# Kernel optimization log

Measured on AMD Instinct MI355X. Metric: run time of the kernel, lower is better.

Reference implementation:

```python
import jax, jax.numpy as jnp
import numpy as np

N, E, G = 50000, 800000, 64
IN, HID, T, EDGE_DIM, HLS = 32, 64, 2, 2, 32
# deg histogram: all nodes degree 16 -> avg_deg['log'] = log(16+1)
AVG_LOG = float(np.log(17.0))


def _pna(x, src, dst, eattr, We, be, Wpre, bpre, Wpost, bpost, Wlin, blin):
    """PNAConv with aggregators [mean,min,max,std], scalers [identity,amp,att],
    towers=T, pre_layers=1, post_layers=1, divide_input=False."""
    n, F = x.shape
    enc = eattr @ We + be                                   # [E, F] edge encoder
    # message: concat(x_i, x_j, edge) -> per-tower Linear(3F -> F)
    h = jnp.concatenate([x[dst], x[src], enc], axis=-1)     # [E, 3F] (same for all towers)
    m = jnp.einsum('ef,tfo->eto', h, Wpre) + bpre           # [E, T, F]
    ones = jnp.ones((m.shape[0],), m.dtype)
    cnt = jax.ops.segment_sum(ones, dst, num_segments=n)    # in-degree [N]
    d = jnp.maximum(cnt, 1.0)[:, None, None]
    s = jax.ops.segment_sum(m, dst, num_segments=n)
    mean = s / d
    msq = jax.ops.segment_sum(m * m, dst, num_segments=n) / d
    std = jnp.sqrt(jax.nn.relu(msq - mean * mean) + 1e-5)
    has = (cnt > 0)[:, None, None]
    mn = jnp.where(has, jax.ops.segment_min(m, dst, num_segments=n), 0.0)
    mx = jnp.where(has, jax.ops.segment_max(m, dst, num_segments=n), 0.0)
    agg = jnp.concatenate([mean, mn, mx, std], axis=-1)     # [N, T, 4F]
    logd = jnp.log(d + 1.0)
    scaled = jnp.concatenate([agg, agg * (logd / AVG_LOG), agg * (AVG_LOG / logd)], axis=-1)  # [N,T,12F]
    xt = jnp.broadcast_to(x[:, None, :], (n, Wpre.shape[0], F))
    out = jnp.concatenate([xt, scaled], axis=-1)            # [N, T, 13F]
    o = jnp.einsum('nti,tio->nto', out, Wpost) + bpost      # [N, T, F_out]
    return o.reshape(n, -1) @ Wlin + blin                   # [N, HID]


def setup_inputs():
    key = jax.random.key(0)
    ks = iter(jax.random.split(key, 48))
    def p(shape):
        return jax.random.normal(next(ks), shape, jnp.float32) * 0.05
    inp = {}
    inp['x'] = jax.random.normal(next(ks), (N, IN), jnp.float32)
    inp['edge_attr'] = jax.random.normal(next(ks), (E, EDGE_DIM), jnp.float32)
    inp['hls_attr'] = jax.random.normal(next(ks), (G, HLS), jnp.float32)
    inp['edge_index'] = jax.random.randint(next(ks), (2, E), 0, N)
    inp['batch'] = jnp.sort(jax.random.randint(next(ks), (N,), 0, G))
    Fo = HID // T
    for l, Fin in enumerate([IN, HID]):
        inp[f'We{l}'] = p((EDGE_DIM, Fin)); inp[f'be{l}'] = jnp.zeros((Fin,), jnp.float32)
        inp[f'Wpre{l}'] = p((T, 3 * Fin, Fin)); inp[f'bpre{l}'] = jnp.zeros((T, Fin), jnp.float32)
        inp[f'Wpost{l}'] = p((T, 13 * Fin, Fo)); inp[f'bpost{l}'] = jnp.zeros((T, Fo), jnp.float32)
        inp[f'Wlin{l}'] = p((HID, HID)); inp[f'blin{l}'] = jnp.zeros((HID,), jnp.float32)
    inp['W1'] = p((HID + HLS, 64)); inp['b1'] = jnp.zeros((64,), jnp.float32)
    inp['W2'] = p((64, 64)); inp['b2'] = jnp.zeros((64,), jnp.float32)
    inp['W3'] = p((64, 1)); inp['b3'] = jnp.zeros((1,), jnp.float32)
    return inp


def reference(x, edge_attr, hls_attr,
              We0, be0, Wpre0, bpre0, Wpost0, bpost0, Wlin0, blin0,
              We1, be1, Wpre1, bpre1, Wpost1, bpost1, Wlin1, blin1,
              W1, b1, W2, b2, W3, b3,
              edge_index, batch):
    src, dst = edge_index[0], edge_index[1]
    h = jax.nn.relu(_pna(x, src, dst, edge_attr, We0, be0, Wpre0, bpre0, Wpost0, bpost0, Wlin0, blin0))
    h = jax.nn.relu(_pna(h, src, dst, edge_attr, We1, be1, Wpre1, bpre1, Wpost1, bpost1, Wlin1, blin1))
    g = jax.ops.segment_sum(h, batch, num_segments=G)       # global_add_pool [G, HID]
    g = jnp.concatenate([g, hls_attr], axis=-1)
    g = jax.nn.relu(g @ W1 + b1)
    g = jax.nn.relu(g @ W2 + b2)
    return g @ W3 + b3                                      # [G, 1]
```

## Files before the change

### kernel.cpp

```cpp
#include <hip/hip_runtime.h>
#include <math.h>
#include <float.h>

#define NN 50000
#define EE 800000
#define CAP 64

#define NB 196
#define SPAN 256
#define BCAP 4608

typedef unsigned short ushort_t;
typedef short short8 __attribute__((ext_vector_type(8)));
typedef float floatx4 __attribute__((ext_vector_type(4)));

__device__ __constant__ float kAVG_LOG = 2.8332133440562162f;

__device__ inline ushort_t f2bf(float v) {
    union { float f; unsigned u; } x; x.f = v;
    unsigned r = x.u + 0x7fffu + ((x.u >> 16) & 1u);
    return (ushort_t)(r >> 16);
}
__device__ inline float bf2f(ushort_t b) {
    union { unsigned u; float f; } x; x.u = ((unsigned)b) << 16; return x.f;
}
__device__ inline float bitsf(unsigned u) {
    union { unsigned u; float f; } x; x.u = u; return x.f;
}
__device__ inline void splitbf(float v, ushort_t& hi, ushort_t& lo) {
    hi = f2bf(v);
    lo = f2bf(v - bf2f(hi));
}

template <int F>
__device__ void prep_ab_dev(const float* __restrict__ We, const float* __restrict__ be,
                            const float* __restrict__ Wpre, const float* __restrict__ bpre,
                            float* __restrict__ U, float* __restrict__ Wab,
                            float* __restrict__ bias_ab) {
    const int TF = 2 * F;
    int tid = threadIdx.x;
    for (int idx = tid; idx < 2 * TF; idx += 256) {
        int c = idx / TF, f = idx % TF;
        int t = f / F, o = f % F;
        float s = 0.f;
        for (int g = 0; g < F; ++g)
            s += We[c * F + g] * Wpre[((size_t)t * 3 * F + 2 * F + g) * F + o];
        U[idx] = s;
    }
    for (int idx = tid; idx < F * 2 * TF; idx += 256) {
        int g = idx / (2 * TF), cc = idx % (2 * TF);
        int t, o, row;
        if (cc < TF) { t = cc / F; o = cc % F; row = g; }
        else { int c2 = cc - TF; t = c2 / F; o = c2 % F; row = F + g; }
        Wab[idx] = Wpre[((size_t)t * 3 * F + row) * F + o];
    }
    for (int cc = tid; cc < 2 * TF; cc += 256) {
        float v = 0.f;
        if (cc < TF) {
            int t = cc / F, o = cc % F;
            float s = 0.f;
            for (int g = 0; g < F; ++g)
                s += be[g] * Wpre[((size_t)t * 3 * F + 2 * F + g) * F + o];
            v = s + bpre[t * F + o];
        }
        bias_ab[cc] = v;
    }
}

template <int F>
__device__ void prep_zf_elem(int idx, const float* __restrict__ Wpost, const float* __restrict__ Wlin,
                             ushort_t* __restrict__ Bh, ushort_t* __restrict__ Bl) {
    const int KT = 9 * F;
    int jg = idx / KT, k = idx - jg * KT;
    int b = jg >> 6, j = jg & 63;
    float v = 0.f;
    if (k < F) {
        if (b == 0) {
#pragma unroll
            for (int t = 0; t < 2; ++t)
#pragma unroll
                for (int c = 0; c < 32; ++c)
                    v += Wpost[((size_t)t * 13 * F + k) * 32 + c] * Wlin[(t * 32 + c) * 64 + j];
        }
    } else {
        int r = k - F;
        int t = r / (4 * F), rr = r - t * 4 * F;
#pragma unroll
        for (int c = 0; c < 32; ++c)
            v += Wpost[((size_t)t * 13 * F + F + b * 4 * F + rr) * 32 + c] * Wlin[(t * 32 + c) * 64 + j];
    }
    ushort_t h_, l_;
    splitbf(v, h_, l_);
    Bh[(size_t)jg * KT + k] = h_;
    Bl[(size_t)jg * KT + k] = l_;
}

#define NZ0 216
#define NZ1 432
#define PREPB (NZ0 + NZ1 + 3)
#define INITB 6250

__global__ __launch_bounds__(256) void prep_init(
    const float* We0, const float* be0, const float* Wpre0, const float* bpre0,
    const float* Wpost0, const float* Wlin0, const float* bpost0, const float* blin0,
    const float* We1, const float* be1, const float* Wpre1, const float* bpre1,
    const float* Wpost1, const float* Wlin1, const float* bpost1, const float* blin1,
    float* U0, float* Wab0, float* bias_ab0, ushort_t* Bh0, ushort_t* Bl0, float* bias_zf0,
    float* U1, float* Wab1, float* bias_ab1, ushort_t* Bh1, ushort_t* Bl1, float* bias_zf1,
    int* gcount, float* pool, const float* __restrict__ x, ushort_t* __restrict__ xb) {
    int b = blockIdx.x;
    int tid = threadIdx.x;
    if (b >= PREPB) {
        int i = (b - PREPB) * 256 + tid;
        if (i < NN * 32) xb[i] = f2bf(x[i]);
        if (i < NB) gcount[i] = 0;
        if (i < 64 * 64) pool[i] = 0.f;
        return;
    }
    if (b < NZ0) {
        prep_zf_elem<32>(b * 256 + tid, Wpost0, Wlin0, Bh0, Bl0);
    } else if (b < NZ0 + NZ1) {
        prep_zf_elem<64>((b - NZ0) * 256 + tid, Wpost1, Wlin1, Bh1, Bl1);
    } else if (b == NZ0 + NZ1) {
        prep_ab_dev<32>(We0, be0, Wpre0, bpre0, U0, Wab0, bias_ab0);
    } else if (b == NZ0 + NZ1 + 1) {
        prep_ab_dev<64>(We1, be1, Wpre1, bpre1, U1, Wab1, bias_ab1);
    } else {
        for (int j = tid; j < 64; j += 256) {
            float s0 = blin0[j], s1 = blin1[j];
#pragma unroll
            for (int t = 0; t < 2; ++t)
#pragma unroll
                for (int c = 0; c < 32; ++c) {
                    s0 += bpost0[t * 32 + c] * Wlin0[(t * 32 + c) * 64 + j];
                    s1 += bpost1[t * 32 + c] * Wlin1[(t * 32 + c) * 64 + j];
                }
            bias_zf0[j] = s0;
            bias_zf1[j] = s1;
        }
    }
}

__global__ __launch_bounds__(1024) void partition_edges(
    const int* __restrict__ ei, const float* __restrict__ ea,
    int* __restrict__ gcount, uint2* __restrict__ part) {
    __shared__ int hist[NB];
    __shared__ int lbase[NB];
    int tid = threadIdx.x;
    int e0 = blockIdx.x * 4096;
    for (int i = tid; i < NB; i += 1024) hist[i] = 0;
    __syncthreads();
    int bq[4], rnk[4];
    unsigned px[4], py[4];
#pragma unroll
    for (int q = 0; q < 4; ++q) {
        int e = e0 + q * 1024 + tid;
        bq[q] = -1;
        if (e < EE) {
            int s = ei[e];
            int d = ei[EE + e];
            float2 v = *(const float2*)(ea + 2 * e);
            bq[q] = d >> 8;
            px[q] = ((unsigned)(d & 255) << 16) | (unsigned)s;
            py[q] = ((unsigned)f2bf(v.y) << 16) | (unsigned)f2bf(v.x);
            rnk[q] = atomicAdd(&hist[bq[q]], 1);
        }
    }
    __syncthreads();
    for (int i = tid; i < NB; i += 1024)
        lbase[i] = atomicAdd(&gcount[i], hist[i]);
    __syncthreads();
#pragma unroll
    for (int q = 0; q < 4; ++q) {
        if (bq[q] >= 0) {
            int slot = lbase[bq[q]] + rnk[q];
            if (slot < BCAP)
                part[(size_t)bq[q] * BCAP + slot] = make_uint2(px[q], py[q]);
        }
    }
}

__device__ void csr_fill_block(int g, const int* __restrict__ gcount,
                               const uint2* __restrict__ part,
                               int* __restrict__ cnt, uint2* __restrict__ csr) {
    __shared__ int lcnt[SPAN];
    int tid = threadIdx.x;
    lcnt[tid] = 0;
    __syncthreads();
    int total = gcount[g];
    if (total > BCAP) total = BCAP;
    size_t pbase = (size_t)g * BCAP;
    for (int i = tid; i < total; i += 256) {
        uint2 rec = part[pbase + i];
        int rel = rec.x >> 16;
        int src = rec.x & 0xffff;
        int p = atomicAdd(&lcnt[rel], 1);
        if (p < CAP) {
            int node = (g << 8) + rel;
            csr[(size_t)node * CAP + p] = make_uint2((unsigned)src, rec.y);
        }
    }
    __syncthreads();
    int node = (g << 8) + tid;
    if (node < NN) cnt[node] = lcnt[tid];
}

__device__ void gemm_bias_block(const float* __restrict__ A, const float* __restrict__ B,
                                const float* __restrict__ bias, float* __restrict__ Ca,
                                ushort_t* __restrict__ Cb, int M, int K, int Ncols, int bstart,
                                int mb, int cb) {
    __shared__ float As[32][132];
    __shared__ float Bs[32][68];
    int m0 = mb * 128, c0 = cb * 64;
    int tid = threadIdx.x;
    int tx = tid & 15, ty = tid >> 4;
    int ms = tid >> 3, u = tid & 7;
    float acc[8][4] = {};
    for (int k0 = 0; k0 < K; k0 += 32) {
#pragma unroll
        for (int p = 0; p < 4; ++p) {
            int m = ms + 32 * p;
            int gm = m0 + m;
            float4 v = make_float4(0.f, 0.f, 0.f, 0.f);
            if (gm < M) v = *(const float4*)(A + (size_t)gm * K + k0 + u * 4);
            As[u * 4 + 0][m] = v.x; As[u * 4 + 1][m] = v.y;
            As[u * 4 + 2][m] = v.z; As[u * 4 + 3][m] = v.w;
        }
#pragma unroll
        for (int p = 0; p < 2; ++p) {
            int idx = tid + 256 * p;
            int kk = idx >> 4, q = idx & 15;
            *(float4*)&Bs[kk][q * 4] = *(const float4*)(B + (size_t)(k0 + kk) * Ncols + c0 + q * 4);
        }
        __syncthreads();
#pragma unroll 8
        for (int k = 0; k < 32; ++k) {
            float a0[8], b0[4];
            *(float4*)&a0[0] = *(const float4*)&As[k][ty * 8];
            *(float4*)&a0[4] = *(const float4*)&As[k][ty * 8 + 4];
            *(float4*)&b0[0] = *(const float4*)&Bs[k][tx * 4];
#pragma unroll
            for (int i = 0; i < 8; ++i)
#pragma unroll
                for (int j = 0; j < 4; ++j) acc[i][j] = fmaf(a0[i], b0[j], acc[i][j]);
        }
        __syncthreads();
    }
    float bj[4];
#pragma unroll
    for (int j = 0; j < 4; ++j) bj[j] = bias[c0 + tx * 4 + j];
    bool bside = (c0 >= bstart);
    int TFw = bstart;
#pragma unroll
    for (int i = 0; i < 8; ++i) {
        int gm = m0 + ty * 8 + i;
        if (gm >= M) continue;
        float v0 = acc[i][0] + bj[0], v1 = acc[i][1] + bj[1];
        float v2 = acc[i][2] + bj[2], v3 = acc[i][3] + bj[3];
        if (!bside) {
            *(float4*)(Ca + (size_t)gm * TFw + c0 + tx * 4) = make_float4(v0, v1, v2, v3);
        } else {
            ushort4 w;
            w.x = f2bf(v0); w.y = f2bf(v1); w.z = f2bf(v2); w.w = f2bf(v3);
            *(ushort4*)(Cb + (size_t)gm * TFw + (c0 - bstart) + tx * 4) = w;
        }
    }
}

__global__ __launch_bounds__(256) void gemm_bias(const float* __restrict__ A, const float* __restrict__ B,
                                                 const float* __restrict__ bias, float* __restrict__ Ca,
                                                 ushort_t* __restrict__ Cb, int M, int K, int Ncols, int bstart) {
    gemm_bias_block(A, B, bias, Ca, Cb, M, K, Ncols, bstart, blockIdx.x, blockIdx.y);
}

__global__ __launch_bounds__(256) void csr_gemm0(
    const int* __restrict__ gcount, const uint2* __restrict__ part,
    int* __restrict__ cnt, uint2* __restrict__ csr,
    const float* __restrict__ A, const float* __restrict__ B, const float* __restrict__ bias,
    float* __restrict__ Ca, ushort_t* __restrict__ Cb) {
    int bx = blockIdx.x;
    if (bx % 5 == 0) {
        csr_fill_block(bx / 5, gcount, part, cnt, csr);
    } else {
        int idx = bx - 1 - bx / 5;
        gemm_bias_block(A, B, bias, Ca, Cb, NN, 32, 128, 64, idx % 391, idx / 391);
    }
}

template <int F>
__global__ __launch_bounds__(256) void aggregate(const float* __restrict__ ABa, const ushort_t* __restrict__ ABb,
                                                 const int* __restrict__ cnt, const uint2* __restrict__ csr,
                                                 const float* __restrict__ U,
                                                 ushort_t* __restrict__ agg_b, float2* __restrict__ sc) {
    const int TF = 2 * F;
    const int FPL = TF / 64;
    int lane = threadIdx.x & 63;
    int n = blockIdx.x * 4 + (threadIdx.x >> 6);
    if (n >= NN) return;
    int f0 = FPL * lane;

    float base[FPL], u0[FPL], u1[FPL], sum[FPL], sq[FPL], mn[FPL], mx[FPL];
#pragma unroll
    for (int r = 0; r < FPL; ++r) {
        base[r] = ABa[(size_t)n * TF + f0 + r];
        u0[r] = U[f0 + r];
        u1[r] = U[TF + f0 + r];
        sum[r] = 0.f; sq[r] = 0.f; mn[r] = FLT_MAX; mx[r] = -FLT_MAX;
    }
    int deg = cnt[n];
    int ec = deg < CAP ? deg : CAP;
    if (ec > 0) {
        int ebase = n * CAP;
        int myi = lane < ec ? lane : ec - 1;
        uint2 ent = csr[ebase + myi];
        int msrc = (int)ent.x;
        unsigned mea = ent.y;
        int e = 0;
        for (; e + 8 <= ec; e += 8) {
            int sb[8]; unsigned ep[8];
            unsigned wv[8];
#pragma unroll
            for (int i = 0; i < 8; ++i) {
                sb[i] = __shfl(msrc, e + i);
                ep[i] = (unsigned)__shfl((int)mea, e + i);
            }
#pragma unroll
            for (int i = 0; i < 8; ++i) {
                if constexpr (FPL == 2)
                    wv[i] = *(const unsigned*)(ABb + (size_t)sb[i] * TF + f0);
                else
                    wv[i] = ABb[(size_t)sb[i] * TF + f0];
            }
#pragma unroll
            for (int i = 0; i < 8; ++i) {
                float ex = bitsf(ep[i] << 16);
                float ey = bitsf(ep[i] & 0xffff0000u);
                float v[FPL];
                if constexpr (FPL == 2) {
                    v[0] = bitsf(wv[i] << 16);
                    v[1] = bitsf(wv[i] & 0xffff0000u);
                } else {
                    v[0] = bitsf(wv[i] << 16);
                }
#pragma unroll
                for (int r = 0; r < FPL; ++r) {
                    float q = fmaf(ex, u0[r], fmaf(ey, u1[r], v[r]));
                    sum[r] += q;
                    sq[r] = fmaf(q, q, sq[r]);
                    mn[r] = fminf(mn[r], q);
                    mx[r] = fmaxf(mx[r], q);
                }
            }
        }
        if (e < ec) {
            int sb[8]; unsigned ep[8];
            unsigned wv[8];
#pragma unroll
            for (int i = 0; i < 8; ++i) {
                sb[i] = __shfl(msrc, e + i);
                ep[i] = (unsigned)__shfl((int)mea, e + i);
            }
#pragma unroll
            for (int i = 0; i < 8; ++i) {
                if (e + i < ec) {
                    if constexpr (FPL == 2)
                        wv[i] = *(const unsigned*)(ABb + (size_t)sb[i] * TF + f0);
                    else
                        wv[i] = ABb[(size_t)sb[i] * TF + f0];
                }
            }
#pragma unroll
            for (int i = 0; i < 8; ++i) {
                if (e + i < ec) {
                    float ex = bitsf(ep[i] << 16);
                    float ey = bitsf(ep[i] & 0xffff0000u);
                    float v[FPL];
                    if constexpr (FPL == 2) {
                        v[0] = bitsf(wv[i] << 16);
                        v[1] = bitsf(wv[i] & 0xffff0000u);
                    } else {
                        v[0] = bitsf(wv[i] << 16);
                    }
#pragma unroll
                    for (int r = 0; r < FPL; ++r) {
                        float q = fmaf(ex, u0[r], fmaf(ey, u1[r], v[r]));
                        sum[r] += q;
                        sq[r] = fmaf(q, q, sq[r]);
                        mn[r] = fminf(mn[r], q);
                        mx[r] = fmaxf(mx[r], q);
                    }
                }
            }
        }
    }
    float d = (float)(deg > 1 ? deg : 1);
    float inv_d = 1.f / d;
    bool has = deg > 0;
#pragma unroll
    for (int r = 0; r < FPL; ++r) {
        float mean_q = sum[r] * inv_d;
        float var = sq[r] * inv_d - mean_q * mean_q;
        float stdv = sqrtf(fmaxf(var, 0.f) + 1e-5f);
        float mean = has ? base[r] + mean_q : 0.f;
        float vmn = has ? base[r] + mn[r] : 0.f;
        float vmx = has ? base[r] + mx[r] : 0.f;
        int f = f0 + r;
        int t = f / F, o = f - t * F;
        size_t rowb = (size_t)n * (4 * TF) + (size_t)t * (4 * F);
        agg_b[rowb + o] = f2bf(mean);
        agg_b[rowb + F + o] = f2bf(vmn);
        agg_b[rowb + 2 * F + o] = f2bf(vmx);
        agg_b[rowb + 3 * F + o] = f2bf(stdv);
    }
    if (lane == 0) {
        float logd = logf(d + 1.f);
        sc[n] = make_float2(logd / kAVG_LOG, kAVG_LOG / logd);
    }
}

template <int F, bool POOL>
__global__ __launch_bounds__(256, 2) void gemm_zf(
    const ushort_t* __restrict__ xs_b, const ushort_t* __restrict__ agg_b,
    const ushort_t* __restrict__ Bh, const ushort_t* __restrict__ Bl,
    const float* __restrict__ bias_zf, const float2* __restrict__ sc,
    float* __restrict__ H, ushort_t* __restrict__ H_b,
    const int* __restrict__ batch, float* __restrict__ pool) {
    const int KT = 9 * F;
    extern __shared__ char smem[];
    ushort_t* A_s  = (ushort_t*)smem;
    ushort_t* Bh_s = A_s + 128 * 40;
    ushort_t* Bl_s = Bh_s + 192 * 40;
    float* hbuf = (float*)smem;

    int m0 = blockIdx.x * 128;
    int tid = threadIdx.x;
    int lane = tid & 63;
    int wave = tid >> 6;
    int ln = lane & 15, quad = lane >> 4;

    floatx4 acc[8][3];
#pragma unroll
    for (int i = 0; i < 8; ++i)
#pragma unroll
        for (int j = 0; j < 3; ++j) acc[i][j] = (floatx4)(0.f);

    int arow = tid >> 2, asg = tid & 3;
    int bcol[3], bsg[3];
#pragma unroll
    for (int p = 0; p < 3; ++p) {
        int idx = tid + 256 * p;
        bcol[p] = idx >> 2;
        bsg[p] = idx & 3;
    }

    const short8 zero8 = {0, 0, 0, 0, 0, 0, 0, 0};
    short8 pa[2], pbh[3], pbl[3];
    {
        int c0 = asg * 8;
#pragma unroll
        for (int q = 0; q < 2; ++q) {
            int gm = m0 + arow + q * 64;
            pa[q] = zero8;
            if (gm < NN) pa[q] = *(const short8*)(xs_b + (size_t)gm * F + c0);
        }
#pragma unroll
        for (int p = 0; p < 3; ++p) {
            pbh[p] = *(const short8*)(Bh + (size_t)bcol[p] * KT + bsg[p] * 8);
            pbl[p] = *(const short8*)(Bl + (size_t)bcol[p] * KT + bsg[p] * 8);
        }
    }

    for (int k0 = 0; k0 < KT; k0 += 32) {
#pragma unroll
        for (int q = 0; q < 2; ++q)
            *(short8*)&A_s[(arow + q * 64) * 40 + asg * 8] = pa[q];
#pragma unroll
        for (int p = 0; p < 3; ++p) {
            *(short8*)&Bh_s[bcol[p] * 40 + bsg[p] * 8] = pbh[p];
            *(short8*)&Bl_s[bcol[p] * 40 + bsg[p] * 8] = pbl[p];
        }
        __syncthreads();
        short8 bh[3], bl[3];
#pragma unroll
        for (int b = 0; b < 3; ++b) {
            int col = b * 64 + wave * 16 + ln;
            bh[b] = *(short8*)&Bh_s[col * 40 + quad * 8];
            bl[b] = *(short8*)&Bl_s[col * 40 + quad * 8];
        }
        int kn = k0 + 32;
        if (kn < KT) {
            int c0 = kn + asg * 8;
#pragma unroll
            for (int q = 0; q < 2; ++q) {
                int gm = m0 + arow + q * 64;
                pa[q] = zero8;
                if (gm < NN) {
                    pa[q] = (c0 < F) ? *(const short8*)(xs_b + (size_t)gm * F + c0)
                                     : *(const short8*)(agg_b + (size_t)gm * 8 * F + (c0 - F));
                }
            }
#pragma unroll
            for (int p = 0; p < 3; ++p) {
                pbh[p] = *(const short8*)(Bh + (size_t)bcol[p] * KT + kn + bsg[p] * 8);
                pbl[p] = *(const short8*)(Bl + (size_t)bcol[p] * KT + kn + bsg[p] * 8);
            }
        }
#pragma unroll
        for (int rf = 0; rf < 8; ++rf) {
            short8 ah = *(short8*)&A_s[(rf * 16 + ln) * 40 + quad * 8];
#pragma unroll
            for (int b = 0; b < 3; ++b) {
                acc[rf][b] = __builtin_amdgcn_mfma_f32_16x16x32_bf16(ah, bh[b], acc[rf][b], 0, 0, 0);
                acc[rf][b] = __builtin_amdgcn_mfma_f32_16x16x32_bf16(ah, bl[b], acc[rf][b], 0, 0, 0);
            }
        }
        __syncthreads();
    }

    int ocol = wave * 16 + ln;
    float bcolv = bias_zf[ocol];

    if (POOL) __syncthreads();

#pragma unroll
    for (int rf = 0; rf < 8; ++rf) {
#pragma unroll
        for (int reg = 0; reg < 4; ++reg) {
            int r = rf * 16 + quad * 4 + reg;
            int gm = m0 + r;
            float2 s = make_float2(0.f, 0.f);
            if (gm < NN) s = sc[gm];
            float y = acc[rf][0][reg] + s.x * acc[rf][1][reg] + s.y * acc[rf][2][reg] + bcolv;
            y = fmaxf(y, 0.f);
            if (POOL) {
                hbuf[r * 68 + ocol] = (gm < NN) ? y : 0.f;
            } else if (gm < NN) {
                H[(size_t)gm * 64 + ocol] = y;
                H_b[(size_t)gm * 64 + ocol] = f2bf(y);
            }
        }
    }
    if (POOL) {
        __syncthreads();
        int col = tid & 63, grp = tid >> 6;
        float a = 0.f;
        int cur = -1;
        for (int i = 0; i < 32; ++i) {
            int r = grp * 32 + i;
            int gm = m0 + r;
            if (gm >= NN) break;
            int b = batch[gm];
            if (b != cur) {
                if (cur >= 0) atomicAdd(&pool[cur * 64 + col], a);
                cur = b; a = 0.f;
            }
            a += hbuf[r * 68 + col];
        }
        if (cur >= 0) atomicAdd(&pool[cur * 64 + col], a);
    }
}

__global__ __launch_bounds__(256) void head_kernel(const float* __restrict__ gpool, const float* __restrict__ hls,
                                                   const float* __restrict__ W1, const float* __restrict__ b1,
                                                   const float* __restrict__ W2, const float* __restrict__ b2,
                                                   const float* __restrict__ W3, const float* __restrict__ b3,
                                                   float* __restrict__ out) {
    __shared__ float gin[64][96];
    __shared__ float r1[64][64];
    __shared__ float r2[64][64];
    int tid = threadIdx.x;
    for (int idx = tid; idx < 64 * 96; idx += 256) {
        int g = idx / 96, j = idx % 96;
        gin[g][j] = (j < 64) ? gpool[g * 64 + j] : hls[g * 32 + (j - 64)];
    }
    __syncthreads();
    for (int idx = tid; idx < 64 * 64; idx += 256) {
        int g = idx / 64, j = idx % 64;
        float acc = b1[j];
        for (int k = 0; k < 96; ++k) acc = fmaf(gin[g][k], W1[k * 64 + j], acc);
        r1[g][j] = fmaxf(acc, 0.f);
    }
    __syncthreads();
    for (int idx = tid; idx < 64 * 64; idx += 256) {
        int g = idx / 64, j = idx % 64;
        float acc = b2[j];
        for (int k = 0; k < 64; ++k) acc = fmaf(r1[g][k], W2[k * 64 + j], acc);
        r2[g][j] = fmaxf(acc, 0.f);
    }
    __syncthreads();
    if (tid < 64) {
        float acc = b3[0];
        for (int k = 0; k < 64; ++k) acc = fmaf(r2[tid][k], W3[k], acc);
        out[tid] = acc;
    }
}

extern "C" void kernel_launch(void* const* d_in, const int* in_sizes, int n_in,
                              void* d_out, int out_size, void* d_ws, size_t ws_size,
                              hipStream_t stream) {
    (void)in_sizes; (void)n_in; (void)out_size; (void)ws_size;
    const float* x     = (const float*)d_in[0];
    const float* eattr = (const float*)d_in[1];
    const float* hls   = (const float*)d_in[2];
    const int*   eidx  = (const int*)d_in[3];
    const int*   batch = (const int*)d_in[4];
    const float* We[2]    = {(const float*)d_in[5],  (const float*)d_in[13]};
    const float* be[2]    = {(const float*)d_in[6],  (const float*)d_in[14]};
    const float* Wpre[2]  = {(const float*)d_in[7],  (const float*)d_in[15]};
    const float* bpre[2]  = {(const float*)d_in[8],  (const float*)d_in[16]};
    const float* Wpost[2] = {(const float*)d_in[9],  (const float*)d_in[17]};
    const float* bpost[2] = {(const float*)d_in[10], (const float*)d_in[18]};
    const float* Wlin[2]  = {(const float*)d_in[11], (const float*)d_in[19]};
    const float* blin[2]  = {(const float*)d_in[12], (const float*)d_in[20]};
    const float* W1 = (const float*)d_in[21]; const float* b1 = (const float*)d_in[22];
    const float* W2 = (const float*)d_in[23]; const float* b2 = (const float*)d_in[24];
    const float* W3 = (const float*)d_in[25]; const float* b3 = (const float*)d_in[26];
    float* out = (float*)d_out;

    char* ws = (char*)d_ws;
    size_t off = 0;
    auto carve = [&](size_t bytes) -> char* {
        char* p = ws + off;
        off = (off + bytes + 255) & ~(size_t)255;
        return p;
    };
    int*      cnt      = (int*)carve((size_t)NN * 4);
    uint2*    csr      = (uint2*)carve((size_t)NN * CAP * 8);
    float*    ABa      = (float*)carve((size_t)NN * 128 * 4);
    ushort_t* ABb      = (ushort_t*)carve((size_t)NN * 128 * 2);
    ushort_t* agg_b    = (ushort_t*)carve((size_t)NN * 512 * 2);
    float2*   sc       = (float2*)carve((size_t)NN * 8);
    ushort_t* xs_b     = (ushort_t*)carve((size_t)NN * 32 * 2);
    float*    h1       = (float*)carve((size_t)NN * 64 * 4);
    ushort_t* h1_b     = (ushort_t*)carve((size_t)NN * 64 * 2);
    float*    U0       = (float*)carve(256 * 4);
    float*    U1       = (float*)carve(256 * 4);
    float*    Wab0     = (float*)carve(16384 * 4);
    float*    Wab1     = (float*)carve(16384 * 4);
    float*    bias_ab0 = (float*)carve(256 * 4);
    float*    bias_ab1 = (float*)carve(256 * 4);
    ushort_t* Bh0      = (ushort_t*)carve((size_t)192 * 288 * 2);
    ushort_t* Bl0      = (ushort_t*)carve((size_t)192 * 288 * 2);
    ushort_t* Bh1      = (ushort_t*)carve((size_t)192 * 576 * 2);
    ushort_t* Bl1      = (ushort_t*)carve((size_t)192 * 576 * 2);
    float*    bias_zf0 = (float*)carve(64 * 4);
    float*    bias_zf1 = (float*)carve(64 * 4);
    float*    pool     = (float*)carve(64 * 64 * 4);
    int*      gcount   = (int*)carve(NB * 4);
    uint2*    part     = (uint2*)agg_b;

    const int MB128 = (NN + 127) / 128;
    const int SMEM_ZF = (128 * 40 + 192 * 40 + 192 * 40) * 2;
    const int FUSEDB = NB + MB128 * 2;

    prep_init<<<PREPB + INITB, 256, 0, stream>>>(
        We[0], be[0], Wpre[0], bpre[0], Wpost[0], Wlin[0], bpost[0], blin[0],
        We[1], be[1], Wpre[1], bpre[1], Wpost[1], Wlin[1], bpost[1], blin[1],
        U0, Wab0, bias_ab0, Bh0, Bl0, bias_zf0,
        U1, Wab1, bias_ab1, Bh1, Bl1, bias_zf1,
        gcount, pool, x, xs_b);

    partition_edges<<<(EE + 4095) / 4096, 1024, 0, stream>>>(eidx, eattr, gcount, part);

    csr_gemm0<<<FUSEDB, 256, 0, stream>>>(gcount, part, cnt, csr, x, Wab0, bias_ab0, ABa, ABb);
    aggregate<32><<<(NN + 3) / 4, 256, 0, stream>>>(ABa, ABb, cnt, csr, U0, agg_b, sc);
    gemm_zf<32, false><<<MB128, 256, SMEM_ZF, stream>>>(xs_b, agg_b, Bh0, Bl0, bias_zf0, sc,
                                                        h1, h1_b, batch, pool);

    gemm_bias<<<dim3(MB128, 4), 256, 0, stream>>>(h1, Wab1, bias_ab1, ABa, ABb, NN, 64, 256, 128);
    aggregate<64><<<(NN + 3) / 4, 256, 0, stream>>>(ABa, ABb, cnt, csr, U1, agg_b, sc);
    gemm_zf<64, true><<<MB128, 256, SMEM_ZF, stream>>>(h1_b, agg_b, Bh1, Bl1, bias_zf1, sc,
                                                       nullptr, nullptr, batch, pool);

    head_kernel<<<1, 256, 0, stream>>>(pool, hls, W1, b1, W2, b2, W3, b3, out);
}
```

Measured before the change: 330.1 us.

## Fuse layer-1 edge GEMM into layer-0 post GEMM and scalarize CSR reads

The layer-0 post-aggregation GEMM now keeps its ReLU output tile in shared memory and immediately multiplies it by the layer-1 message weights. It writes ABa/ABb directly, which removes the separate gemm_bias launch and the fp32 h1 round trip through global memory. The aggregate kernel also makes the node index wave-uniform and loads CSR entries as vector loads, replacing the per-lane load plus shuffle broadcast. The cost is more shared memory and serial work at the end of each gemm_zf block.

Result: no change. 332.3 us (+0.6%).

```diff
diff --git a/kernel.cpp b/kernel.cpp
--- a/kernel.cpp
+++ b/kernel.cpp
@@ -267,12 +267,6 @@
     }
 }
 
-__global__ __launch_bounds__(256) void gemm_bias(const float* __restrict__ A, const float* __restrict__ B,
-                                                 const float* __restrict__ bias, float* __restrict__ Ca,
-                                                 ushort_t* __restrict__ Cb, int M, int K, int Ncols, int bstart) {
-    gemm_bias_block(A, B, bias, Ca, Cb, M, K, Ncols, bstart, blockIdx.x, blockIdx.y);
-}
-
 __global__ __launch_bounds__(256) void csr_gemm0(
     const int* __restrict__ gcount, const uint2* __restrict__ part,
     int* __restrict__ cnt, uint2* __restrict__ csr,
@@ -297,6 +291,7 @@
     int lane = threadIdx.x & 63;
     int n = blockIdx.x * 4 + (threadIdx.x >> 6);
     if (n >= NN) return;
+    n = __builtin_amdgcn_readfirstlane(n);
     int f0 = FPL * lane;
 
     float base[FPL], u0[FPL], u1[FPL], sum[FPL], sq[FPL], mn[FPL], mx[FPL];
@@ -309,90 +304,71 @@
     }
     int deg = cnt[n];
     int ec = deg < CAP ? deg : CAP;
-    if (ec > 0) {
-        int ebase = n * CAP;
-        int myi = lane < ec ? lane : ec - 1;
-        uint2 ent = csr[ebase + myi];
-        int msrc = (int)ent.x;
-        unsigned mea = ent.y;
-        int e = 0;
-        for (; e + 8 <= ec; e += 8) {
-            int sb[8]; unsigned ep[8];
-            unsigned wv[8];
-#pragma unroll
-            for (int i = 0; i < 8; ++i) {
-                sb[i] = __shfl(msrc, e + i);
-                ep[i] = (unsigned)__shfl((int)mea, e + i);
-            }
-#pragma unroll
-            for (int i = 0; i < 8; ++i) {
-                if constexpr (FPL == 2)
-                    wv[i] = *(const unsigned*)(ABb + (size_t)sb[i] * TF + f0);
-                else
-                    wv[i] = ABb[(size_t)sb[i] * TF + f0];
-            }
-#pragma unroll
-            for (int i = 0; i < 8; ++i) {
-                float ex = bitsf(ep[i] << 16);
-                float ey = bitsf(ep[i] & 0xffff0000u);
-                float v[FPL];
-                if constexpr (FPL == 2) {
-                    v[0] = bitsf(wv[i] << 16);
-                    v[1] = bitsf(wv[i] & 0xffff0000u);
-                } else {
-                    v[0] = bitsf(wv[i] << 16);
-                }
-#pragma unroll
-                for (int r = 0; r < FPL; ++r) {
-                    float q = fmaf(ex, u0[r], fmaf(ey, u1[r], v[r]));
-                    sum[r] += q;
-                    sq[r] = fmaf(q, q, sq[r]);
-                    mn[r] = fminf(mn[r], q);
-                    mx[r] = fmaxf(mx[r], q);
-                }
-            }
-        }
-        if (e < ec) {
-            int sb[8]; unsigned ep[8];
-            unsigned wv[8];
-#pragma unroll
-            for (int i = 0; i < 8; ++i) {
-                sb[i] = __shfl(msrc, e + i);
-                ep[i] = (unsigned)__shfl((int)mea, e + i);
-            }
-#pragma unroll
-            for (int i = 0; i < 8; ++i) {
-                if (e + i < ec) {
-                    if constexpr (FPL == 2)
-                        wv[i] = *(const unsigned*)(ABb + (size_t)sb[i] * TF + f0);
-                    else
-                        wv[i] = ABb[(size_t)sb[i] * TF + f0];
-                }
-            }
-#pragma unroll
-            for (int i = 0; i < 8; ++i) {
-                if (e + i < ec) {
-                    float ex = bitsf(ep[i] << 16);
-                    float ey = bitsf(ep[i] & 0xffff0000u);
-                    float v[FPL];
-                    if constexpr (FPL == 2) {
-                        v[0] = bitsf(wv[i] << 16);
-                        v[1] = bitsf(wv[i] & 0xffff0000u);
-                    } else {
-                        v[0] = bitsf(wv[i] << 16);
-                    }
-#pragma unroll
-                    for (int r = 0; r < FPL; ++r) {
-                        float q = fmaf(ex, u0[r], fmaf(ey, u1[r], v[r]));
-                        sum[r] += q;
-                        sq[r] = fmaf(q, q, sq[r]);
-                        mn[r] = fminf(mn[r], q);
-                        mx[r] = fmaxf(mx[r], q);
-                    }
-                }
-            }
-        }
-    }
+    const uint2* __restrict__ p = csr + (size_t)n * CAP;
+
+    int e = 0;
+    for (; e + 8 <= ec; e += 8) {
+        uint4 c0 = *(const uint4*)(p + e);
+        uint4 c1 = *(const uint4*)(p + e + 2);
+        uint4 c2 = *(const uint4*)(p + e + 4);
+        uint4 c3 = *(const uint4*)(p + e + 6);
+        unsigned sb[8] = {c0.x, c0.z, c1.x, c1.z, c2.x, c2.z, c3.x, c3.z};
+        unsigned ep[8] = {c0.y, c0.w, c1.y, c1.w, c2.y, c2.w, c3.y, c3.w};
+        unsigned wv[8];
+#pragma unroll
+        for (int i = 0; i < 8; ++i) {
+            const ushort_t* row = ABb + (size_t)sb[i] * TF;
+            if constexpr (FPL == 2)
+                wv[i] = *(const unsigned*)(row + f0);
+            else
+                wv[i] = row[f0];
+        }
+#pragma unroll
+        for (int i = 0; i < 8; ++i) {
+            float ex = bitsf(ep[i] << 16);
+            float ey = bitsf(ep[i] & 0xffff0000u);
+            float v[FPL];
+            if constexpr (FPL == 2) {
+                v[0] = bitsf(wv[i] << 16);
+                v[1] = bitsf(wv[i] & 0xffff0000u);
+            } else {
+                v[0] = bitsf(wv[i] << 16);
+            }
+#pragma unroll
+            for (int r = 0; r < FPL; ++r) {
+                float q = fmaf(ex, u0[r], fmaf(ey, u1[r], v[r]));
+                sum[r] += q;
+                sq[r] = fmaf(q, q, sq[r]);
+                mn[r] = fminf(mn[r], q);
+                mx[r] = fmaxf(mx[r], q);
+            }
+        }
+    }
+    for (; e < ec; ++e) {
+        uint2 ent = p[e];
+        const ushort_t* row = ABb + (size_t)ent.x * TF;
+        unsigned wvt;
+        if constexpr (FPL == 2) wvt = *(const unsigned*)(row + f0);
+        else wvt = row[f0];
+        float ex = bitsf(ent.y << 16);
+        float ey = bitsf(ent.y & 0xffff0000u);
+        float v[FPL];
+        if constexpr (FPL == 2) {
+            v[0] = bitsf(wvt << 16);
+            v[1] = bitsf(wvt & 0xffff0000u);
+        } else {
+            v[0] = bitsf(wvt << 16);
+        }
+#pragma unroll
+        for (int r = 0; r < FPL; ++r) {
+            float q = fmaf(ex, u0[r], fmaf(ey, u1[r], v[r]));
+            sum[r] += q;
+            sq[r] = fmaf(q, q, sq[r]);
+            mn[r] = fminf(mn[r], q);
+            mx[r] = fmaxf(mx[r], q);
+        }
+    }
+
     float d = (float)(deg > 1 ? deg : 1);
     float inv_d = 1.f / d;
     bool has = deg > 0;
@@ -418,19 +394,22 @@
     }
 }
 
-template <int F, bool POOL>
+template <int F, bool POOL, bool FUSEAB>
 __global__ __launch_bounds__(256, 2) void gemm_zf(
     const ushort_t* __restrict__ xs_b, const ushort_t* __restrict__ agg_b,
     const ushort_t* __restrict__ Bh, const ushort_t* __restrict__ Bl,
     const float* __restrict__ bias_zf, const float2* __restrict__ sc,
-    float* __restrict__ H, ushort_t* __restrict__ H_b,
-    const int* __restrict__ batch, float* __restrict__ pool) {
+    ushort_t* __restrict__ H_b,
+    const int* __restrict__ batch, float* __restrict__ pool,
+    const float* __restrict__ Wab_n, const float* __restrict__ bias_ab_n,
+    float* __restrict__ ABa, ushort_t* __restrict__ ABb) {
     const int KT = 9 * F;
     extern __shared__ char smem[];
     ushort_t* A_s  = (ushort_t*)smem;
     ushort_t* Bh_s = A_s + 128 * 40;
     ushort_t* Bl_s = Bh_s + 192 * 40;
     float* hbuf = (float*)smem;
+    float* h1s  = (float*)smem;
 
     int m0 = blockIdx.x * 128;
     int tid = threadIdx.x;
@@ -534,9 +513,9 @@
             y = fmaxf(y, 0.f);
             if (POOL) {
                 hbuf[r * 68 + ocol] = (gm < NN) ? y : 0.f;
-            } else if (gm < NN) {
-                H[(size_t)gm * 64 + ocol] = y;
-                H_b[(size_t)gm * 64 + ocol] = f2bf(y);
+            } else {
+                if (gm < NN) H_b[(size_t)gm * 64 + ocol] = f2bf(y);
+                if (FUSEAB) h1s[ocol * 132 + r] = (gm < NN) ? y : 0.f;
             }
         }
     }
@@ -557,6 +536,54 @@
             a += hbuf[r * 68 + col];
         }
         if (cur >= 0) atomicAdd(&pool[cur * 64 + col], a);
+    }
+    if (FUSEAB) {
+        __syncthreads();
+        float* Bs2 = (float*)(smem + 64 * 132 * 4);
+        int tx = tid & 15, ty = tid >> 4;
+        for (int cb = 0; cb < 4; ++cb) {
+            int c0 = cb * 64;
+            float a2[8][4] = {};
+            for (int k0 = 0; k0 < 64; k0 += 32) {
+#pragma unroll
+                for (int pp = 0; pp < 2; ++pp) {
+                    int idx = tid + 256 * pp;
+                    int kk = idx >> 4, q = idx & 15;
+                    *(float4*)&Bs2[kk * 68 + q * 4] =
+                        *(const float4*)(Wab_n + (size_t)(k0 + kk) * 256 + c0 + q * 4);
+                }
+                __syncthreads();
+#pragma unroll 8
+                for (int k = 0; k < 32; ++k) {
+                    float a0[8], b0[4];
+                    *(float4*)&a0[0] = *(const float4*)&h1s[(k0 + k) * 132 + ty * 8];
+                    *(float4*)&a0[4] = *(const float4*)&h1s[(k0 + k) * 132 + ty * 8 + 4];
+                    *(float4*)&b0[0] = *(const float4*)&Bs2[k * 68 + tx * 4];
+#pragma unroll
+                    for (int i = 0; i < 8; ++i)
+#pragma unroll
+                        for (int j = 0; j < 4; ++j) a2[i][j] = fmaf(a0[i], b0[j], a2[i][j]);
+                }
+                __syncthreads();
+            }
+            float bj[4];
+#pragma unroll
+            for (int j = 0; j < 4; ++j) bj[j] = bias_ab_n[c0 + tx * 4 + j];
+#pragma unroll
+            for (int i = 0; i < 8; ++i) {
+                int gm = m0 + ty * 8 + i;
+                if (gm >= NN) continue;
+                float v0 = a2[i][0] + bj[0], v1 = a2[i][1] + bj[1];
+                float v2 = a2[i][2] + bj[2], v3 = a2[i][3] + bj[3];
+                if (cb < 2) {
+                    *(float4*)(ABa + (size_t)gm * 128 + c0 + tx * 4) = make_float4(v0, v1, v2, v3);
+                } else {
+                    ushort4 w;
+                    w.x = f2bf(v0); w.y = f2bf(v1); w.z = f2bf(v2); w.w = f2bf(v3);
+                    *(ushort4*)(ABb + (size_t)gm * 128 + (c0 - 128) + tx * 4) = w;
+                }
+            }
+        }
     }
 }
 
@@ -631,7 +658,6 @@
     ushort_t* agg_b    = (ushort_t*)carve((size_t)NN * 512 * 2);
     float2*   sc       = (float2*)carve((size_t)NN * 8);
     ushort_t* xs_b     = (ushort_t*)carve((size_t)NN * 32 * 2);
-    float*    h1       = (float*)carve((size_t)NN * 64 * 4);
     ushort_t* h1_b     = (ushort_t*)carve((size_t)NN * 64 * 2);
     float*    U0       = (float*)carve(256 * 4);
     float*    U1       = (float*)carve(256 * 4);
@@ -650,7 +676,8 @@
     uint2*    part     = (uint2*)agg_b;
 
     const int MB128 = (NN + 127) / 128;
-    const int SMEM_ZF = (128 * 40 + 192 * 40 + 192 * 40) * 2;
+    const int SMEM_ZF   = (128 * 40 + 192 * 40 + 192 * 40) * 2;
+    const int SMEM_ZF32 = 64 * 132 * 4 + 32 * 68 * 4;
     const int FUSEDB = NB + MB128 * 2;
 
     prep_init<<<PREPB + INITB, 256, 0, stream>>>(
@@ -664,13 +691,14 @@
 
     csr_gemm0<<<FUSEDB, 256, 0, stream>>>(gcount, part, cnt, csr, x, Wab0, bias_ab0, ABa, ABb);
     aggregate<32><<<(NN + 3) / 4, 256, 0, stream>>>(ABa, ABb, cnt, csr, U0, agg_b, sc);
-    gemm_zf<32, false><<<MB128, 256, SMEM_ZF, stream>>>(xs_b, agg_b, Bh0, Bl0, bias_zf0, sc,
-                                                        h1, h1_b, batch, pool);
-
-    gemm_bias<<<dim3(MB128, 4), 256, 0, stream>>>(h1, Wab1, bias_ab1, ABa, ABb, NN, 64, 256, 128);
+    gemm_zf<32, false, true><<<MB128, 256, SMEM_ZF32, stream>>>(
+        xs_b, agg_b, Bh0, Bl0, bias_zf0, sc, h1_b, batch, pool,
+        Wab1, bias_ab1, ABa, ABb);
+
     aggregate<64><<<(NN + 3) / 4, 256, 0, stream>>>(ABa, ABb, cnt, csr, U1, agg_b, sc);
-    gemm_zf<64, true><<<MB128, 256, SMEM_ZF, stream>>>(h1_b, agg_b, Bh1, Bl1, bias_zf1, sc,
-                                                       nullptr, nullptr, batch, pool);
+    gemm_zf<64, true, false><<<MB128, 256, SMEM_ZF, stream>>>(
+        h1_b, agg_b, Bh1, Bl1, bias_zf1, sc, nullptr, batch, pool,
+        nullptr, nullptr, nullptr, nullptr);
 
     head_kernel<<<1, 256, 0, stream>>>(pool, hls, W1, b1, W2, b2, W3, b3, out);
 }
```

## Use scalar CSR loads in aggregate and halve gemm_zf row tile

Applied to the files above, without the earlier changes.

The aggregate kernel makes the node index wave-uniform with readfirstlane. It then reads CSR entries directly as uint4 loads, which the compiler can turn into scalar loads, replacing the per-lane load plus shuffle broadcast. The masked remainder block becomes a simple scalar tail loop. gemm_zf drops from 128 to 64 rows per block, with fewer accumulators, a smaller LDS footprint and launch bounds raised to 4 blocks per CU, to get more blocks and occupancy. The __syncthreads before the pool staging buffer, which aliases the A/B tiles in shared memory, is removed, so there is a risk of a shared-memory race.

Measured after the change: 349.9 us. 1.06x slower.

```diff
diff --git a/kernel.cpp b/kernel.cpp
--- a/kernel.cpp
+++ b/kernel.cpp
@@ -297,6 +297,7 @@
     int lane = threadIdx.x & 63;
     int n = blockIdx.x * 4 + (threadIdx.x >> 6);
     if (n >= NN) return;
+    n = __builtin_amdgcn_readfirstlane(n);
     int f0 = FPL * lane;
 
     float base[FPL], u0[FPL], u1[FPL], sum[FPL], sq[FPL], mn[FPL], mx[FPL];
@@ -309,90 +310,71 @@
     }
     int deg = cnt[n];
     int ec = deg < CAP ? deg : CAP;
-    if (ec > 0) {
-        int ebase = n * CAP;
-        int myi = lane < ec ? lane : ec - 1;
-        uint2 ent = csr[ebase + myi];
-        int msrc = (int)ent.x;
-        unsigned mea = ent.y;
-        int e = 0;
-        for (; e + 8 <= ec; e += 8) {
-            int sb[8]; unsigned ep[8];
-            unsigned wv[8];
-#pragma unroll
-            for (int i = 0; i < 8; ++i) {
-                sb[i] = __shfl(msrc, e + i);
-                ep[i] = (unsigned)__shfl((int)mea, e + i);
+    const uint2* __restrict__ p = csr + (size_t)n * CAP;
+
+    int e = 0;
+    for (; e + 8 <= ec; e += 8) {
+        uint4 c0 = *(const uint4*)(p + e);
+        uint4 c1 = *(const uint4*)(p + e + 2);
+        uint4 c2 = *(const uint4*)(p + e + 4);
+        uint4 c3 = *(const uint4*)(p + e + 6);
+        unsigned sb[8] = {c0.x, c0.z, c1.x, c1.z, c2.x, c2.z, c3.x, c3.z};
+        unsigned ep[8] = {c0.y, c0.w, c1.y, c1.w, c2.y, c2.w, c3.y, c3.w};
+        unsigned wv[8];
+#pragma unroll
+        for (int i = 0; i < 8; ++i) {
+            const ushort_t* row = ABb + (size_t)sb[i] * TF;
+            if constexpr (FPL == 2)
+                wv[i] = *(const unsigned*)(row + f0);
+            else
+                wv[i] = row[f0];
+        }
+#pragma unroll
+        for (int i = 0; i < 8; ++i) {
+            float ex = bitsf(ep[i] << 16);
+            float ey = bitsf(ep[i] & 0xffff0000u);
+            float v[FPL];
+            if constexpr (FPL == 2) {
+                v[0] = bitsf(wv[i] << 16);
+                v[1] = bitsf(wv[i] & 0xffff0000u);
+            } else {
+                v[0] = bitsf(wv[i] << 16);
             }
 #pragma unroll
-            for (int i = 0; i < 8; ++i) {
-                if constexpr (FPL == 2)
-                    wv[i] = *(const unsigned*)(ABb + (size_t)sb[i] * TF + f0);
-                else
-                    wv[i] = ABb[(size_t)sb[i] * TF + f0];
+            for (int r = 0; r < FPL; ++r) {
+                float q = fmaf(ex, u0[r], fmaf(ey, u1[r], v[r]));
+                sum[r] += q;
+                sq[r] = fmaf(q, q, sq[r]);
+                mn[r] = fminf(mn[r], q);
+                mx[r] = fmaxf(mx[r], q);
             }
-#pragma unroll
-            for (int i = 0; i < 8; ++i) {
-                float ex = bitsf(ep[i] << 16);
-                float ey = bitsf(ep[i] & 0xffff0000u);
-                float v[FPL];
-                if constexpr (FPL == 2) {
-                    v[0] = bitsf(wv[i] << 16);
-                    v[1] = bitsf(wv[i] & 0xffff0000u);
-                } else {
-                    v[0] = bitsf(wv[i] << 16);
-                }
-#pragma unroll
-                for (int r = 0; r < FPL; ++r) {
-                    float q = fmaf(ex, u0[r], fmaf(ey, u1[r], v[r]));
-                    sum[r] += q;
-                    sq[r] = fmaf(q, q, sq[r]);
-                    mn[r] = fminf(mn[r], q);
-                    mx[r] = fmaxf(mx[r], q);
-                }
-            }
-        }
-        if (e < ec) {
-            int sb[8]; unsigned ep[8];
-            unsigned wv[8];
-#pragma unroll
-            for (int i = 0; i < 8; ++i) {
-                sb[i] = __shfl(msrc, e + i);
-                ep[i] = (unsigned)__shfl((int)mea, e + i);
-            }
-#pragma unroll
-            for (int i = 0; i < 8; ++i) {
-                if (e + i < ec) {
-                    if constexpr (FPL == 2)
-                        wv[i] = *(const unsigned*)(ABb + (size_t)sb[i] * TF + f0);
-                    else
-                        wv[i] = ABb[(size_t)sb[i] * TF + f0];
-                }
-            }
-#pragma unroll
-            for (int i = 0; i < 8; ++i) {
-                if (e + i < ec) {
-                    float ex = bitsf(ep[i] << 16);
-                    float ey = bitsf(ep[i] & 0xffff0000u);
-                    float v[FPL];
-                    if constexpr (FPL == 2) {
-                        v[0] = bitsf(wv[i] << 16);
-                        v[1] = bitsf(wv[i] & 0xffff0000u);
-                    } else {
-                        v[0] = bitsf(wv[i] << 16);
-                    }
-#pragma unroll
-                    for (int r = 0; r < FPL; ++r) {
-                        float q = fmaf(ex, u0[r], fmaf(ey, u1[r], v[r]));
-                        sum[r] += q;
-                        sq[r] = fmaf(q, q, sq[r]);
-                        mn[r] = fminf(mn[r], q);
-                        mx[r] = fmaxf(mx[r], q);
-                    }
-                }
-            }
-        }
-    }
+        }
+    }
+    for (; e < ec; ++e) {
+        uint2 ent = p[e];
+        const ushort_t* row = ABb + (size_t)ent.x * TF;
+        unsigned wvt;
+        if constexpr (FPL == 2) wvt = *(const unsigned*)(row + f0);
+        else wvt = row[f0];
+        float ex = bitsf(ent.y << 16);
+        float ey = bitsf(ent.y & 0xffff0000u);
+        float v[FPL];
+        if constexpr (FPL == 2) {
+            v[0] = bitsf(wvt << 16);
+            v[1] = bitsf(wvt & 0xffff0000u);
+        } else {
+            v[0] = bitsf(wvt << 16);
+        }
+#pragma unroll
+        for (int r = 0; r < FPL; ++r) {
+            float q = fmaf(ex, u0[r], fmaf(ey, u1[r], v[r]));
+            sum[r] += q;
+            sq[r] = fmaf(q, q, sq[r]);
+            mn[r] = fminf(mn[r], q);
+            mx[r] = fmaxf(mx[r], q);
+        }
+    }
+
     float d = (float)(deg > 1 ? deg : 1);
     float inv_d = 1.f / d;
     bool has = deg > 0;
@@ -419,7 +401,7 @@
 }
 
 template <int F, bool POOL>
-__global__ __launch_bounds__(256, 2) void gemm_zf(
+__global__ __launch_bounds__(256, 4) void gemm_zf(
     const ushort_t* __restrict__ xs_b, const ushort_t* __restrict__ agg_b,
     const ushort_t* __restrict__ Bh, const ushort_t* __restrict__ Bl,
     const float* __restrict__ bias_zf, const float2* __restrict__ sc,
@@ -428,19 +410,19 @@
     const int KT = 9 * F;
     extern __shared__ char smem[];
     ushort_t* A_s  = (ushort_t*)smem;
-    ushort_t* Bh_s = A_s + 128 * 40;
+    ushort_t* Bh_s = A_s + 64 * 40;
     ushort_t* Bl_s = Bh_s + 192 * 40;
     float* hbuf = (float*)smem;
 
-    int m0 = blockIdx.x * 128;
+    int m0 = blockIdx.x * 64;
     int tid = threadIdx.x;
     int lane = tid & 63;
     int wave = tid >> 6;
     int ln = lane & 15, quad = lane >> 4;
 
-    floatx4 acc[8][3];
-#pragma unroll
-    for (int i = 0; i < 8; ++i)
+    floatx4 acc[4][3];
+#pragma unroll
+    for (int i = 0; i < 4; ++i)
 #pragma unroll
         for (int j = 0; j < 3; ++j) acc[i][j] = (floatx4)(0.f);
 
@@ -454,15 +436,12 @@
     }
 
     const short8 zero8 = {0, 0, 0, 0, 0, 0, 0, 0};
-    short8 pa[2], pbh[3], pbl[3];
+    short8 pa, pbh[3], pbl[3];
     {
         int c0 = asg * 8;
-#pragma unroll
-        for (int q = 0; q < 2; ++q) {
-            int gm = m0 + arow + q * 64;
-            pa[q] = zero8;
-            if (gm < NN) pa[q] = *(const short8*)(xs_b + (size_t)gm * F + c0);
-        }
+        int gm = m0 + arow;
+        pa = zero8;
+        if (gm < NN) pa = *(const short8*)(xs_b + (size_t)gm * F + c0);
 #pragma unroll
         for (int p = 0; p < 3; ++p) {
             pbh[p] = *(const short8*)(Bh + (size_t)bcol[p] * KT + bsg[p] * 8);
@@ -471,9 +450,7 @@
     }
 
     for (int k0 = 0; k0 < KT; k0 += 32) {
-#pragma unroll
-        for (int q = 0; q < 2; ++q)
-            *(short8*)&A_s[(arow + q * 64) * 40 + asg * 8] = pa[q];
+        *(short8*)&A_s[arow * 40 + asg * 8] = pa;
 #pragma unroll
         for (int p = 0; p < 3; ++p) {
             *(short8*)&Bh_s[bcol[p] * 40 + bsg[p] * 8] = pbh[p];
@@ -490,14 +467,11 @@
         int kn = k0 + 32;
         if (kn < KT) {
             int c0 = kn + asg * 8;
-#pragma unroll
-            for (int q = 0; q < 2; ++q) {
-                int gm = m0 + arow + q * 64;
-                pa[q] = zero8;
-                if (gm < NN) {
-                    pa[q] = (c0 < F) ? *(const short8*)(xs_b + (size_t)gm * F + c0)
-                                     : *(const short8*)(agg_b + (size_t)gm * 8 * F + (c0 - F));
-                }
+            int gm = m0 + arow;
+            pa = zero8;
+            if (gm < NN) {
+                pa = (c0 < F) ? *(const short8*)(xs_b + (size_t)gm * F + c0)
+                              : *(const short8*)(agg_b + (size_t)gm * 8 * F + (c0 - F));
             }
 #pragma unroll
             for (int p = 0; p < 3; ++p) {
@@ -506,7 +480,7 @@
             }
         }
 #pragma unroll
-        for (int rf = 0; rf < 8; ++rf) {
+        for (int rf = 0; rf < 4; ++rf) {
             short8 ah = *(short8*)&A_s[(rf * 16 + ln) * 40 + quad * 8];
 #pragma unroll
             for (int b = 0; b < 3; ++b) {
@@ -520,10 +494,8 @@
     int ocol = wave * 16 + ln;
     float bcolv = bias_zf[ocol];
 
-    if (POOL) __syncthreads();
-
-#pragma unroll
-    for (int rf = 0; rf < 8; ++rf) {
+#pragma unroll
+    for (int rf = 0; rf < 4; ++rf) {
 #pragma unroll
         for (int reg = 0; reg < 4; ++reg) {
             int r = rf * 16 + quad * 4 + reg;
@@ -545,8 +517,8 @@
         int col = tid & 63, grp = tid >> 6;
         float a = 0.f;
         int cur = -1;
-        for (int i = 0; i < 32; ++i) {
-            int r = grp * 32 + i;
+        for (int i = 0; i < 16; ++i) {
+            int r = grp * 16 + i;
             int gm = m0 + r;
             if (gm >= NN) break;
             int b = batch[gm];
@@ -650,7 +622,8 @@
     uint2*    part     = (uint2*)agg_b;
 
     const int MB128 = (NN + 127) / 128;
-    const int SMEM_ZF = (128 * 40 + 192 * 40 + 192 * 40) * 2;
+    const int MB64  = (NN + 63) / 64;
+    const int SMEM_ZF = (64 * 40 + 192 * 40 + 192 * 40) * 2;
     const int FUSEDB = NB + MB128 * 2;
 
     prep_init<<<PREPB + INITB, 256, 0, stream>>>(
@@ -664,13 +637,13 @@
 
     csr_gemm0<<<FUSEDB, 256, 0, stream>>>(gcount, part, cnt, csr, x, Wab0, bias_ab0, ABa, ABb);
     aggregate<32><<<(NN + 3) / 4, 256, 0, stream>>>(ABa, ABb, cnt, csr, U0, agg_b, sc);
-    gemm_zf<32, false><<<MB128, 256, SMEM_ZF, stream>>>(xs_b, agg_b, Bh0, Bl0, bias_zf0, sc,
-                                                        h1, h1_b, batch, pool);
+    gemm_zf<32, false><<<MB64, 256, SMEM_ZF, stream>>>(xs_b, agg_b, Bh0, Bl0, bias_zf0, sc,
+                                                       h1, h1_b, batch, pool);
 
     gemm_bias<<<dim3(MB128, 4), 256, 0, stream>>>(h1, Wab1, bias_ab1, ABa, ABb, NN, 64, 256, 128);
     aggregate<64><<<(NN + 3) / 4, 256, 0, stream>>>(ABa, ABb, cnt, csr, U1, agg_b, sc);
-    gemm_zf<64, true><<<MB128, 256, SMEM_ZF, stream>>>(h1_b, agg_b, Bh1, Bl1, bias_zf1, sc,
-                                                       nullptr, nullptr, batch, pool);
+    gemm_zf<64, true><<<MB64, 256, SMEM_ZF, stream>>>(h1_b, agg_b, Bh1, Bl1, bias_zf1, sc,
+                                                      nullptr, nullptr, batch, pool);
 
     head_kernel<<<1, 256, 0, stream>>>(pool, hls, W1, b1, W2, b2, W3, b3, out);
 }
```
